# Kernel tuning notes

Measured on AMD Instinct MI355X. Metric: run time of the kernel, lower is better.

The kernel has to match this reference:

```python
import jax, jax.numpy as jnp
import numpy as np

H = W = 32
CROP = int(H * 0.8)  # 25, matches int(H*crop_ratio) in torch
MEAN = jnp.array([0.5071, 0.4867, 0.4408], jnp.float32).reshape(1, 3, 1, 1)
STD = jnp.array([0.2675, 0.2565, 0.2761], jnp.float32).reshape(1, 3, 1, 1)


def _bilinear(img, iy, ix):
    # img [C,H,W]; iy/ix [H,W] float pixel coords (reflected+clamped already)
    y0 = jnp.floor(iy); x0 = jnp.floor(ix)
    wy = iy - y0; wx = ix - x0
    y0i = jnp.clip(y0.astype(jnp.int32), 0, H - 1); y1i = jnp.clip(y0i + 1, 0, H - 1)
    x0i = jnp.clip(x0.astype(jnp.int32), 0, W - 1); x1i = jnp.clip(x0i + 1, 0, W - 1)
    v00 = img[:, y0i, x0i]; v01 = img[:, y0i, x1i]
    v10 = img[:, y1i, x0i]; v11 = img[:, y1i, x1i]
    return v00 * (1 - wy) * (1 - wx) + v01 * (1 - wy) * wx + v10 * wy * (1 - wx) + v11 * wy * wx


def _reflect(c, size):
    # PyTorch grid_sample reflection padding, align_corners=False (reflect about -0.5 / size-0.5)
    lo = -0.5
    span = float(size)
    t = jnp.abs(c - lo)
    extra = jnp.mod(t, span)
    flips = jnp.floor(t / span)
    out = jnp.where(jnp.mod(flips, 2.0) == 0.0, lo + extra, lo + span - extra)
    return jnp.clip(out, 0.0, size - 1.0)


def _crop_resize_one(img, top, left):
    # bilinear resize of img[:, top:top+CROP, left:left+CROP] -> HxW, align_corners=False
    d = (jnp.arange(W, dtype=jnp.float32) + 0.5) * (CROP / W) - 0.5
    d = jnp.maximum(d, 0.0)
    i0 = jnp.floor(d).astype(jnp.int32)
    lam = d - i0
    i1 = jnp.minimum(i0 + 1, CROP - 1)
    r0 = top + i0; r1 = top + i1; c0 = left + i0; c1 = left + i1
    v00 = img[:, r0[:, None], c0[None, :]]
    v01 = img[:, r0[:, None], c1[None, :]]
    v10 = img[:, r1[:, None], c0[None, :]]
    v11 = img[:, r1[:, None], c1[None, :]]
    ly = lam[:, None]; lx = lam[None, :]
    return v00 * (1 - ly) * (1 - lx) + v01 * (1 - ly) * lx + v10 * ly * (1 - lx) + v11 * ly * lx


def _grid_sample_one(img, theta):
    # affine_grid + grid_sample (bilinear, reflection, align_corners=False)
    xs = (2.0 * (jnp.arange(W, dtype=jnp.float32) + 0.5) / W) - 1.0
    ys = (2.0 * (jnp.arange(H, dtype=jnp.float32) + 0.5) / H) - 1.0
    yn, xn = jnp.meshgrid(ys, xs, indexing='ij')
    gx = theta[0, 0] * xn + theta[0, 1] * yn + theta[0, 2]
    gy = theta[1, 0] * xn + theta[1, 1] * yn + theta[1, 2]
    ix = _reflect(((gx + 1.0) * W - 1.0) * 0.5, W)
    iy = _reflect(((gy + 1.0) * H - 1.0) * 0.5, H)
    return _bilinear(img, iy, ix)


def _augment(x, shared_affine, apply_crop):
    B = x.shape[0]
    ks = jax.random.split(jax.random.key(42), 10)
    x = x * STD + MEAN  # de-normalize
    if apply_crop:
        max_off = H - CROP
        top = jax.random.randint(ks[0], (B,), 0, max_off + 1)
        left = jax.random.randint(ks[1], (B,), 0, max_off + 1)
        x = jax.vmap(_crop_resize_one)(x, top, left)
    flip_mask = jax.random.uniform(ks[2], (B,)) < 0.5
    x = jnp.where(flip_mask[:, None, None, None], x[..., ::-1], x)
    # shared affine is provided -> always applied (torch shared_affine branch)
    x = jax.vmap(_grid_sample_one)(x, shared_affine)
    brightness = 1.0 + (jax.random.uniform(ks[3], (B, 1, 1, 1)) - 0.5) * 0.8
    x = x * brightness
    gray = x.mean(axis=1, keepdims=True)
    contrast = 1.0 + (jax.random.uniform(ks[4], (B, 1, 1, 1)) - 0.5) * 0.8
    x = gray + (x - gray) * contrast
    gray = x.mean(axis=1, keepdims=True)
    saturation = 1.0 + (jax.random.uniform(ks[5], (B, 1, 1, 1)) - 0.5) * 0.8
    x = gray + (x - gray) * saturation
    hue_mask = jax.random.uniform(ks[6], (B,)) < 0.5
    x = jnp.where(hue_mask[:, None, None, None], x[:, ::-1], x)  # BGR swap
    gray_mask = jax.random.uniform(ks[7], (B,)) < 0.2
    x = jnp.where(gray_mask[:, None, None, None], x.mean(axis=1, keepdims=True), x)
    blur_mask = jax.random.uniform(ks[8], (B,)) < 0.5
    xp = jnp.pad(x, ((0, 0), (0, 0), (1, 1), (1, 1)), mode='edge')  # replicate pad
    bl = sum(xp[:, :, i:i + H, j:j + W] for i in range(3) for j in range(3)) / 9.0  # 3x3 box blur
    x = jnp.where(blur_mask[:, None, None, None], bl, x)
    solar_mask = jax.random.uniform(ks[9], (B,)) < 0.1
    x = jnp.where(solar_mask[:, None, None, None] & (x > 0.5), 1.0 - x, x)
    x = jnp.clip(x, 0.0, 1.0)
    x = (x - MEAN) / STD  # re-normalize
    return x, flip_mask


def setup_inputs() -> dict:
    key = jax.random.key(0)
    k1, k2 = jax.random.split(key)
    B = 8192
    x = jax.random.normal(k1, (B, 3, H, W), jnp.float32)
    eye = jnp.broadcast_to(jnp.array([[1.0, 0.0, 0.0], [0.0, 1.0, 0.0]], jnp.float32), (B, 2, 3))
    shared_affine = eye + 0.1 * jax.random.normal(k2, (B, 2, 3), jnp.float32)
    return {"x": x, "shared_affine": shared_affine, "apply_crop": 1}


def reference(x, shared_affine, apply_crop):
    out, flip_mask = _augment(x, shared_affine, int(apply_crop))
    # torch returns (x, {'flip': flip_mask, 'affine': affine_theta})
    return out, flip_mask, shared_affine
```

## Files before the change

kernel.cpp:

```cpp
#include <hip/hip_runtime.h>

#define HW 32
#define NPIX 1024
#define IMG 3072

typedef float vf4 __attribute__((ext_vector_type(4)));

__device__ __forceinline__ unsigned rotl32(unsigned x, int d) {
    return (x << d) | (x >> (32 - d));
}

struct UPair { unsigned a, b; };

__device__ __forceinline__ UPair threefry2x32(unsigned k0, unsigned k1,
                                              unsigned x0, unsigned x1) {
    unsigned k2 = k0 ^ k1 ^ 0x1BD11BDAu;
    x0 += k0; x1 += k1;
#define RND(r) { x0 += x1; x1 = rotl32(x1, (r)); x1 ^= x0; }
    RND(13) RND(15) RND(26) RND(6)
    x0 += k1; x1 += k2 + 1u;
    RND(17) RND(29) RND(16) RND(24)
    x0 += k2; x1 += k0 + 2u;
    RND(13) RND(15) RND(26) RND(6)
    x0 += k0; x1 += k1 + 3u;
    RND(17) RND(29) RND(16) RND(24)
    x0 += k1; x1 += k2 + 4u;
    RND(13) RND(15) RND(26) RND(6)
    x0 += k2; x1 += k0 + 5u;
#undef RND
    return {x0, x1};
}

__device__ __forceinline__ float bits_to_u01(unsigned bits) {
    return __uint_as_float((bits >> 9) | 0x3f800000u) - 1.0f;
}

__device__ __forceinline__ float reflect32(float c) {
    float t = fabsf(c + 0.5f);
    float flips = floorf(t * 0.03125f);
    float extra = fmaf(flips, -32.0f, t);
    float o = (((int)flips) & 1) ? (31.5f - extra) : (extra - 0.5f);
    return fminf(fmaxf(o, 0.0f), 31.0f);
}

__device__ __forceinline__ float rfl_f(float v) {
    return __uint_as_float(__builtin_amdgcn_readfirstlane(__float_as_uint(v)));
}
__device__ __forceinline__ int rfl_i(int v) {
    return __builtin_amdgcn_readfirstlane(v);
}

__global__ __launch_bounds__(256) void aug_kernel(
    const float* __restrict__ xin, const float* __restrict__ aff,
    const int* __restrict__ apply_crop, float* __restrict__ out, int B) {
    __shared__ vf4 buf[NPIX];
    __shared__ float s_theta[6];
    __shared__ int s_top, s_left, s_flip, s_hue, s_gray, s_blur, s_solar;
    __shared__ float s_bright, s_contr, s_sat;

    const int b = blockIdx.x;
    const int t = threadIdx.x;
    const int x = t & 31;
    const int yr = t >> 5;
    const bool do_crop = (apply_crop[0] != 0);

    const float* src = xin + (size_t)b * IMG;
    float g0[4], g1[4], g2[4];
#pragma unroll
    for (int i = 0; i < 4; ++i) {
        int p = t + 256 * i;
        g0[i] = src[p];
        g1[i] = src[NPIX + p];
        g2[i] = src[2 * NPIX + p];
    }

    const size_t OUT_IMG = (size_t)B * IMG;
    if (t < 6) {
        float v = aff[b * 6 + t];
        s_theta[t] = v;
        out[OUT_IMG + (size_t)B + (size_t)b * 6 + t] = v;
    }

    if (t < 10) {
        int k = t;
        UPair K = threefry2x32(0u, 42u, 0u, (unsigned)k);
        if (k < 2) {
            UPair k2 = threefry2x32(K.a, K.b, 0u, 1u);
            UPair r = threefry2x32(k2.a, k2.b, 0u, (unsigned)b);
            int val = (int)((r.a ^ r.b) & 7u);
            if (k == 0) s_top = val; else s_left = val;
        } else {
            UPair r = threefry2x32(K.a, K.b, 0u, (unsigned)b);
            float u = bits_to_u01(r.a ^ r.b);
            if      (k == 2) s_flip  = (u < 0.5f);
            else if (k == 3) s_bright = 1.0f + (u - 0.5f) * 0.8f;
            else if (k == 4) s_contr  = 1.0f + (u - 0.5f) * 0.8f;
            else if (k == 5) s_sat    = 1.0f + (u - 0.5f) * 0.8f;
            else if (k == 6) s_hue   = (u < 0.5f);
            else if (k == 7) s_gray  = (u < 0.2f);
            else if (k == 8) s_blur  = (u < 0.5f);
            else             s_solar = (u < 0.1f);
        }
    }

#pragma unroll
    for (int i = 0; i < 4; ++i) {
        vf4 v;
        v.x = fmaf(g0[i], 0.2675f, 0.5071f);
        v.y = fmaf(g1[i], 0.2565f, 0.4867f);
        v.z = fmaf(g2[i], 0.2761f, 0.4408f);
        v.w = 0.0f;
        buf[t + 256 * i] = v;
    }
    __syncthreads();

    if (t == 0) out[OUT_IMG + b] = s_flip ? 1.0f : 0.0f;
    const int top  = rfl_i(s_top),  left = rfl_i(s_left);
    const int flip = rfl_i(s_flip), hue  = rfl_i(s_hue);
    const int gray = rfl_i(s_gray), blur = rfl_i(s_blur), solar = rfl_i(s_solar);
    const float br   = rfl_f(s_bright);
    const float ctsa = rfl_f(s_contr) * rfl_f(s_sat);
    const float th0 = rfl_f(s_theta[0]), th1 = rfl_f(s_theta[1]), th2 = rfl_f(s_theta[2]);
    const float th3 = rfl_f(s_theta[3]), th4 = rfl_f(s_theta[4]), th5 = rfl_f(s_theta[5]);

    float cx[4], cy[4], cz[4];

    if (do_crop) {
        float dxv = fmaxf(fmaf((float)x, 0.78125f, -0.109375f), 0.0f);
        int q0 = (int)dxv; float lx = dxv - (float)q0; int q1 = min(q0 + 1, 24);
        int c0 = left + q0, c1 = left + q1;
        float omx = 1.0f - lx;
#pragma unroll
        for (int i = 0; i < 4; ++i) {
            int yi = yr + 8 * i;
            float dy = fmaxf(fmaf((float)yi, 0.78125f, -0.109375f), 0.0f);
            int i0 = (int)dy; float ly = dy - (float)i0; int i1 = min(i0 + 1, 24);
            int r0 = (top + i0) << 5, r1 = (top + i1) << 5;
            float omy = 1.0f - ly;
            float w00 = omy * omx, w01 = omy * lx;
            float w10 = ly * omx, w11 = ly * lx;
            vf4 t00 = buf[r0 + c0], t01 = buf[r0 + c1];
            vf4 t10 = buf[r1 + c0], t11 = buf[r1 + c1];
            cx[i] = fmaf(t00.x, w00, fmaf(t01.x, w01, fmaf(t10.x, w10, t11.x * w11)));
            cy[i] = fmaf(t00.y, w00, fmaf(t01.y, w01, fmaf(t10.y, w10, t11.y * w11)));
            cz[i] = fmaf(t00.z, w00, fmaf(t01.z, w01, fmaf(t10.z, w10, t11.z * w11)));
        }
        __syncthreads();
#pragma unroll
        for (int i = 0; i < 4; ++i) {
            vf4 v; v.x = cx[i]; v.y = cy[i]; v.z = cz[i]; v.w = 0.0f;
            buf[t + 256 * i] = v;
        }
        __syncthreads();
    }

    {
        float xn = (float)x * 0.0625f - 0.96875f;
#pragma unroll
        for (int i = 0; i < 4; ++i) {
            int yi = yr + 8 * i;
            float yn = (float)yi * 0.0625f - 0.96875f;
            float gx = fmaf(th0, xn, fmaf(th1, yn, th2));
            float gy = fmaf(th3, xn, fmaf(th4, yn, th5));
            float ix = reflect32(fmaf(gx, 16.0f, 15.5f));
            float iy = reflect32(fmaf(gy, 16.0f, 15.5f));
            float fy = floorf(iy), fx = floorf(ix);
            float wy = iy - fy, wx = ix - fx;
            int y0 = (int)fy; int y1 = min(y0 + 1, 31);
            int x0 = (int)fx; int x1 = min(x0 + 1, 31);
            if (flip) { x0 = 31 - x0; x1 = 31 - x1; }
            int r0 = y0 << 5, r1 = y1 << 5;
            float omy = 1.0f - wy, omx = 1.0f - wx;
            float w00 = omy * omx, w01 = omy * wx;
            float w10 = wy * omx, w11 = wy * wx;
            vf4 t00 = buf[r0 + x0], t01 = buf[r0 + x1];
            vf4 t10 = buf[r1 + x0], t11 = buf[r1 + x1];
            float ch0 = fmaf(t00.x, w00, fmaf(t01.x, w01, fmaf(t10.x, w10, t11.x * w11)));
            float ch1 = fmaf(t00.y, w00, fmaf(t01.y, w01, fmaf(t10.y, w10, t11.y * w11)));
            float ch2 = fmaf(t00.z, w00, fmaf(t01.z, w01, fmaf(t10.z, w10, t11.z * w11)));
            ch0 *= br; ch1 *= br; ch2 *= br;
            float g = (ch0 + ch1 + ch2) * (1.0f / 3.0f);
            ch0 = fmaf(ch0 - g, ctsa, g);
            ch1 = fmaf(ch1 - g, ctsa, g);
            ch2 = fmaf(ch2 - g, ctsa, g);
            if (hue) { float tmp = ch0; ch0 = ch2; ch2 = tmp; }
            if (gray) { ch0 = ch1 = ch2 = g; }
            cx[i] = ch0; cy[i] = ch1; cz[i] = ch2;
        }
    }

    if (blur) {
        __syncthreads();
        const int tl = t - 1, tr = t + 1;
        float hx[4], hy[4], hz[4];
#pragma unroll
        for (int i = 0; i < 4; ++i) {
            float v, lf, rt;
            v = cx[i]; lf = __shfl(v, tl); rt = __shfl(v, tr);
            if (x == 0) lf = v;  if (x == 31) rt = v;
            hx[i] = lf + v + rt;
            v = cy[i]; lf = __shfl(v, tl); rt = __shfl(v, tr);
            if (x == 0) lf = v;  if (x == 31) rt = v;
            hy[i] = lf + v + rt;
            v = cz[i]; lf = __shfl(v, tl); rt = __shfl(v, tr);
            if (x == 0) lf = v;  if (x == 31) rt = v;
            hz[i] = lf + v + rt;
        }
#pragma unroll
        for (int i = 0; i < 4; ++i) {
            vf4 v; v.x = hx[i]; v.y = hy[i]; v.z = hz[i]; v.w = 0.0f;
            buf[t + 256 * i] = v;
        }
        __syncthreads();
#pragma unroll
        for (int i = 0; i < 4; ++i) {
            int yi = yr + 8 * i;
            vf4 up = buf[(max(yi - 1, 0) << 5) + x];
            vf4 dn = buf[(min(yi + 1, 31) << 5) + x];
            cx[i] = (up.x + hx[i] + dn.x) * (1.0f / 9.0f);
            cy[i] = (up.y + hy[i] + dn.y) * (1.0f / 9.0f);
            cz[i] = (up.z + hz[i] + dn.z) * (1.0f / 9.0f);
        }
    }

    {
        const float INV0 = 1.0f / 0.2675f, INV1 = 1.0f / 0.2565f, INV2 = 1.0f / 0.2761f;
        float* o = out + (size_t)b * IMG;
#pragma unroll
        for (int i = 0; i < 4; ++i) {
            int p = t + 256 * i;
            float r0v = cx[i], r1v = cy[i], r2v = cz[i];
            if (solar) {
                if (r0v > 0.5f) r0v = 1.0f - r0v;
                if (r1v > 0.5f) r1v = 1.0f - r1v;
                if (r2v > 0.5f) r2v = 1.0f - r2v;
            }
            r0v = fminf(fmaxf(r0v, 0.0f), 1.0f);
            r1v = fminf(fmaxf(r1v, 0.0f), 1.0f);
            r2v = fminf(fmaxf(r2v, 0.0f), 1.0f);
            __builtin_nontemporal_store((r0v - 0.5071f) * INV0, o + p);
            __builtin_nontemporal_store((r1v - 0.4867f) * INV1, o + NPIX + p);
            __builtin_nontemporal_store((r2v - 0.4408f) * INV2, o + 2 * NPIX + p);
        }
    }
}

extern "C" void kernel_launch(void* const* d_in, const int* in_sizes, int n_in,
                              void* d_out, int out_size, void* d_ws, size_t ws_size,
                              hipStream_t stream) {
    const float* x = (const float*)d_in[0];
    const float* aff = (const float*)d_in[1];
    const int* ac = (const int*)d_in[2];
    float* out = (float*)d_out;
    int B = in_sizes[0] / IMG;
    aug_kernel<<<dim3(B), dim3(256), 0, stream>>>(x, aff, ac, out, B);
}
```

Measured before the change: 180.6 us.

## Process four images per block with register prefetch of the next image

Each block now handles four consecutive images in a loop and loads the next image into registers while the current one is processed, so global load latency is hidden. Per-image RNG parameters are computed per wave and broadcast with shuffles instead of going through shared memory, and the crop and grid coordinate constants are hoisted out of the image loop. In exchange the grid shrinks to a quarter of its former size, which lowers the number of waves in flight, and each image still pays for several block barriers.

Result: slower. 206.1 us (+14.1%).

```diff
diff --git a/kernel.cpp b/kernel.cpp
--- a/kernel.cpp
+++ b/kernel.cpp
@@ -3,6 +3,7 @@
 #define HW 32
 #define NPIX 1024
 #define IMG 3072
+#define IPB 4
 
 typedef float vf4 __attribute__((ext_vector_type(4)));
 
@@ -43,125 +44,130 @@
     return fminf(fmaxf(o, 0.0f), 31.0f);
 }
 
-__device__ __forceinline__ float rfl_f(float v) {
-    return __uint_as_float(__builtin_amdgcn_readfirstlane(__float_as_uint(v)));
-}
-__device__ __forceinline__ int rfl_i(int v) {
-    return __builtin_amdgcn_readfirstlane(v);
-}
-
 __global__ __launch_bounds__(256) void aug_kernel(
     const float* __restrict__ xin, const float* __restrict__ aff,
     const int* __restrict__ apply_crop, float* __restrict__ out, int B) {
     __shared__ vf4 buf[NPIX];
-    __shared__ float s_theta[6];
-    __shared__ int s_top, s_left, s_flip, s_hue, s_gray, s_blur, s_solar;
-    __shared__ float s_bright, s_contr, s_sat;
-
-    const int b = blockIdx.x;
+
     const int t = threadIdx.x;
     const int x = t & 31;
     const int yr = t >> 5;
+    const int lane = t & 63;
     const bool do_crop = (apply_crop[0] != 0);
-
-    const float* src = xin + (size_t)b * IMG;
+    const size_t OUT_IMG = (size_t)B * IMG;
+    const int img0 = blockIdx.x * IPB;
+
+    float dxv = fmaxf(fmaf((float)x, 0.78125f, -0.109375f), 0.0f);
+    const int q0c = (int)dxv; const float lxc = dxv - (float)q0c;
+    const int q1c = min(q0c + 1, 24);
+    const float omxc = 1.0f - lxc;
+    const float xn = (float)x * 0.0625f - 0.96875f;
+    int i0a[4], i1a[4]; float lya[4], yna[4];
+#pragma unroll
+    for (int i = 0; i < 4; ++i) {
+        int yi = yr + 8 * i;
+        float dy = fmaxf(fmaf((float)yi, 0.78125f, -0.109375f), 0.0f);
+        i0a[i] = (int)dy; lya[i] = dy - (float)i0a[i];
+        i1a[i] = min(i0a[i] + 1, 24);
+        yna[i] = (float)yi * 0.0625f - 0.96875f;
+    }
+
     float g0[4], g1[4], g2[4];
-#pragma unroll
-    for (int i = 0; i < 4; ++i) {
-        int p = t + 256 * i;
-        g0[i] = src[p];
-        g1[i] = src[NPIX + p];
-        g2[i] = src[2 * NPIX + p];
+    {
+        const float* src = xin + (size_t)img0 * IMG;
+#pragma unroll
+        for (int i = 0; i < 4; ++i) {
+            int p = t + 256 * i;
+            g0[i] = src[p]; g1[i] = src[NPIX + p]; g2[i] = src[2 * NPIX + p];
+        }
     }
 
-    const size_t OUT_IMG = (size_t)B * IMG;
-    if (t < 6) {
-        float v = aff[b * 6 + t];
-        s_theta[t] = v;
-        out[OUT_IMG + (size_t)B + (size_t)b * 6 + t] = v;
-    }
-
-    if (t < 10) {
-        int k = t;
-        UPair K = threefry2x32(0u, 42u, 0u, (unsigned)k);
-        if (k < 2) {
-            UPair k2 = threefry2x32(K.a, K.b, 0u, 1u);
-            UPair r = threefry2x32(k2.a, k2.b, 0u, (unsigned)b);
-            int val = (int)((r.a ^ r.b) & 7u);
-            if (k == 0) s_top = val; else s_left = val;
-        } else {
-            UPair r = threefry2x32(K.a, K.b, 0u, (unsigned)b);
-            float u = bits_to_u01(r.a ^ r.b);
-            if      (k == 2) s_flip  = (u < 0.5f);
-            else if (k == 3) s_bright = 1.0f + (u - 0.5f) * 0.8f;
-            else if (k == 4) s_contr  = 1.0f + (u - 0.5f) * 0.8f;
-            else if (k == 5) s_sat    = 1.0f + (u - 0.5f) * 0.8f;
-            else if (k == 6) s_hue   = (u < 0.5f);
-            else if (k == 7) s_gray  = (u < 0.2f);
-            else if (k == 8) s_blur  = (u < 0.5f);
-            else             s_solar = (u < 0.1f);
-        }
-    }
-
-#pragma unroll
-    for (int i = 0; i < 4; ++i) {
-        vf4 v;
-        v.x = fmaf(g0[i], 0.2675f, 0.5071f);
-        v.y = fmaf(g1[i], 0.2565f, 0.4867f);
-        v.z = fmaf(g2[i], 0.2761f, 0.4408f);
-        v.w = 0.0f;
-        buf[t + 256 * i] = v;
-    }
-    __syncthreads();
-
-    if (t == 0) out[OUT_IMG + b] = s_flip ? 1.0f : 0.0f;
-    const int top  = rfl_i(s_top),  left = rfl_i(s_left);
-    const int flip = rfl_i(s_flip), hue  = rfl_i(s_hue);
-    const int gray = rfl_i(s_gray), blur = rfl_i(s_blur), solar = rfl_i(s_solar);
-    const float br   = rfl_f(s_bright);
-    const float ctsa = rfl_f(s_contr) * rfl_f(s_sat);
-    const float th0 = rfl_f(s_theta[0]), th1 = rfl_f(s_theta[1]), th2 = rfl_f(s_theta[2]);
-    const float th3 = rfl_f(s_theta[3]), th4 = rfl_f(s_theta[4]), th5 = rfl_f(s_theta[5]);
-
-    float cx[4], cy[4], cz[4];
-
-    if (do_crop) {
-        float dxv = fmaxf(fmaf((float)x, 0.78125f, -0.109375f), 0.0f);
-        int q0 = (int)dxv; float lx = dxv - (float)q0; int q1 = min(q0 + 1, 24);
-        int c0 = left + q0, c1 = left + q1;
-        float omx = 1.0f - lx;
+    for (int k = 0; k < IPB; ++k) {
+        const int b = img0 + k;
+        if (b >= B) break;
+
+        float fval = 0.0f; int ival = 0;
+        if (lane < 10) {
+            UPair K = threefry2x32(0u, 42u, 0u, (unsigned)lane);
+            if (lane < 2) {
+                UPair k2 = threefry2x32(K.a, K.b, 0u, 1u);
+                UPair r = threefry2x32(k2.a, k2.b, 0u, (unsigned)b);
+                ival = (int)((r.a ^ r.b) & 7u);
+            } else {
+                UPair r = threefry2x32(K.a, K.b, 0u, (unsigned)b);
+                float u = bits_to_u01(r.a ^ r.b);
+                if      (lane == 2) ival = (u < 0.5f);
+                else if (lane == 3) fval = 1.0f + (u - 0.5f) * 0.8f;
+                else if (lane == 4) fval = 1.0f + (u - 0.5f) * 0.8f;
+                else if (lane == 5) fval = 1.0f + (u - 0.5f) * 0.8f;
+                else if (lane == 6) ival = (u < 0.5f);
+                else if (lane == 7) ival = (u < 0.2f);
+                else if (lane == 8) ival = (u < 0.5f);
+                else                ival = (u < 0.1f);
+            }
+        }
+        const int top  = __shfl(ival, 0), left = __shfl(ival, 1);
+        const int flip = __shfl(ival, 2), hue  = __shfl(ival, 6);
+        const int gray = __shfl(ival, 7), blur = __shfl(ival, 8);
+        const int solar = __shfl(ival, 9);
+        const float br   = __shfl(fval, 3);
+        const float ctsa = __shfl(fval, 4) * __shfl(fval, 5);
+        const float th0 = aff[b * 6 + 0], th1 = aff[b * 6 + 1], th2 = aff[b * 6 + 2];
+        const float th3 = aff[b * 6 + 3], th4 = aff[b * 6 + 4], th5 = aff[b * 6 + 5];
+
 #pragma unroll
         for (int i = 0; i < 4; ++i) {
-            int yi = yr + 8 * i;
-            float dy = fmaxf(fmaf((float)yi, 0.78125f, -0.109375f), 0.0f);
-            int i0 = (int)dy; float ly = dy - (float)i0; int i1 = min(i0 + 1, 24);
-            int r0 = (top + i0) << 5, r1 = (top + i1) << 5;
-            float omy = 1.0f - ly;
-            float w00 = omy * omx, w01 = omy * lx;
-            float w10 = ly * omx, w11 = ly * lx;
-            vf4 t00 = buf[r0 + c0], t01 = buf[r0 + c1];
-            vf4 t10 = buf[r1 + c0], t11 = buf[r1 + c1];
-            cx[i] = fmaf(t00.x, w00, fmaf(t01.x, w01, fmaf(t10.x, w10, t11.x * w11)));
-            cy[i] = fmaf(t00.y, w00, fmaf(t01.y, w01, fmaf(t10.y, w10, t11.y * w11)));
-            cz[i] = fmaf(t00.z, w00, fmaf(t01.z, w01, fmaf(t10.z, w10, t11.z * w11)));
-        }
+            vf4 v;
+            v.x = fmaf(g0[i], 0.2675f, 0.5071f);
+            v.y = fmaf(g1[i], 0.2565f, 0.4867f);
+            v.z = fmaf(g2[i], 0.2761f, 0.4408f);
+            v.w = 0.0f;
+            buf[t + 256 * i] = v;
+        }
+
+        if (k + 1 < IPB && b + 1 < B) {
+            const float* src = xin + (size_t)(b + 1) * IMG;
+#pragma unroll
+            for (int i = 0; i < 4; ++i) {
+                int p = t + 256 * i;
+                g0[i] = src[p]; g1[i] = src[NPIX + p]; g2[i] = src[2 * NPIX + p];
+            }
+        }
+
+        if (t == 0) out[OUT_IMG + b] = flip ? 1.0f : 0.0f;
+        if (t < 6)  out[OUT_IMG + (size_t)B + (size_t)b * 6 + t] = aff[b * 6 + t];
+
         __syncthreads();
+
+        float cx[4], cy[4], cz[4];
+
+        if (do_crop) {
+            const int c0 = left + q0c, c1 = left + q1c;
+#pragma unroll
+            for (int i = 0; i < 4; ++i) {
+                int r0 = (top + i0a[i]) << 5, r1 = (top + i1a[i]) << 5;
+                float ly = lya[i], omy = 1.0f - ly;
+                float w00 = omy * omxc, w01 = omy * lxc;
+                float w10 = ly * omxc, w11 = ly * lxc;
+                vf4 t00 = buf[r0 + c0], t01 = buf[r0 + c1];
+                vf4 t10 = buf[r1 + c0], t11 = buf[r1 + c1];
+                cx[i] = fmaf(t00.x, w00, fmaf(t01.x, w01, fmaf(t10.x, w10, t11.x * w11)));
+                cy[i] = fmaf(t00.y, w00, fmaf(t01.y, w01, fmaf(t10.y, w10, t11.y * w11)));
+                cz[i] = fmaf(t00.z, w00, fmaf(t01.z, w01, fmaf(t10.z, w10, t11.z * w11)));
+            }
+            __syncthreads();
+#pragma unroll
+            for (int i = 0; i < 4; ++i) {
+                vf4 v; v.x = cx[i]; v.y = cy[i]; v.z = cz[i]; v.w = 0.0f;
+                buf[t + 256 * i] = v;
+            }
+            __syncthreads();
+        }
+
 #pragma unroll
         for (int i = 0; i < 4; ++i) {
-            vf4 v; v.x = cx[i]; v.y = cy[i]; v.z = cz[i]; v.w = 0.0f;
-            buf[t + 256 * i] = v;
-        }
-        __syncthreads();
-    }
-
-    {
-        float xn = (float)x * 0.0625f - 0.96875f;
-#pragma unroll
-        for (int i = 0; i < 4; ++i) {
-            int yi = yr + 8 * i;
-            float yn = (float)yi * 0.0625f - 0.96875f;
-            float gx = fmaf(th0, xn, fmaf(th1, yn, th2));
-            float gy = fmaf(th3, xn, fmaf(th4, yn, th5));
+            float gx = fmaf(th0, xn, fmaf(th1, yna[i], th2));
+            float gy = fmaf(th3, xn, fmaf(th4, yna[i], th5));
             float ix = reflect32(fmaf(gx, 16.0f, 15.5f));
             float iy = reflect32(fmaf(gy, 16.0f, 15.5f));
             float fy = floorf(iy), fx = floorf(ix);
@@ -187,61 +193,63 @@
             if (gray) { ch0 = ch1 = ch2 = g; }
             cx[i] = ch0; cy[i] = ch1; cz[i] = ch2;
         }
-    }
-
-    if (blur) {
-        __syncthreads();
-        const int tl = t - 1, tr = t + 1;
-        float hx[4], hy[4], hz[4];
-#pragma unroll
-        for (int i = 0; i < 4; ++i) {
-            float v, lf, rt;
-            v = cx[i]; lf = __shfl(v, tl); rt = __shfl(v, tr);
-            if (x == 0) lf = v;  if (x == 31) rt = v;
-            hx[i] = lf + v + rt;
-            v = cy[i]; lf = __shfl(v, tl); rt = __shfl(v, tr);
-            if (x == 0) lf = v;  if (x == 31) rt = v;
-            hy[i] = lf + v + rt;
-            v = cz[i]; lf = __shfl(v, tl); rt = __shfl(v, tr);
-            if (x == 0) lf = v;  if (x == 31) rt = v;
-            hz[i] = lf + v + rt;
-        }
-#pragma unroll
-        for (int i = 0; i < 4; ++i) {
-            vf4 v; v.x = hx[i]; v.y = hy[i]; v.z = hz[i]; v.w = 0.0f;
-            buf[t + 256 * i] = v;
-        }
-        __syncthreads();
-#pragma unroll
-        for (int i = 0; i < 4; ++i) {
-            int yi = yr + 8 * i;
-            vf4 up = buf[(max(yi - 1, 0) << 5) + x];
-            vf4 dn = buf[(min(yi + 1, 31) << 5) + x];
-            cx[i] = (up.x + hx[i] + dn.x) * (1.0f / 9.0f);
-            cy[i] = (up.y + hy[i] + dn.y) * (1.0f / 9.0f);
-            cz[i] = (up.z + hz[i] + dn.z) * (1.0f / 9.0f);
-        }
-    }
-
-    {
-        const float INV0 = 1.0f / 0.2675f, INV1 = 1.0f / 0.2565f, INV2 = 1.0f / 0.2761f;
-        float* o = out + (size_t)b * IMG;
-#pragma unroll
-        for (int i = 0; i < 4; ++i) {
-            int p = t + 256 * i;
-            float r0v = cx[i], r1v = cy[i], r2v = cz[i];
-            if (solar) {
-                if (r0v > 0.5f) r0v = 1.0f - r0v;
-                if (r1v > 0.5f) r1v = 1.0f - r1v;
-                if (r2v > 0.5f) r2v = 1.0f - r2v;
-            }
-            r0v = fminf(fmaxf(r0v, 0.0f), 1.0f);
-            r1v = fminf(fmaxf(r1v, 0.0f), 1.0f);
-            r2v = fminf(fmaxf(r2v, 0.0f), 1.0f);
-            __builtin_nontemporal_store((r0v - 0.5071f) * INV0, o + p);
-            __builtin_nontemporal_store((r1v - 0.4867f) * INV1, o + NPIX + p);
-            __builtin_nontemporal_store((r2v - 0.4408f) * INV2, o + 2 * NPIX + p);
-        }
+
+        if (blur) {
+            __syncthreads();
+            const int tl = t - 1, tr = t + 1;
+            float hx[4], hy[4], hz[4];
+#pragma unroll
+            for (int i = 0; i < 4; ++i) {
+                float v, lf, rt;
+                v = cx[i]; lf = __shfl(v, tl); rt = __shfl(v, tr);
+                if (x == 0) lf = v;  if (x == 31) rt = v;
+                hx[i] = lf + v + rt;
+                v = cy[i]; lf = __shfl(v, tl); rt = __shfl(v, tr);
+                if (x == 0) lf = v;  if (x == 31) rt = v;
+                hy[i] = lf + v + rt;
+                v = cz[i]; lf = __shfl(v, tl); rt = __shfl(v, tr);
+                if (x == 0) lf = v;  if (x == 31) rt = v;
+                hz[i] = lf + v + rt;
+            }
+#pragma unroll
+            for (int i = 0; i < 4; ++i) {
+                vf4 v; v.x = hx[i]; v.y = hy[i]; v.z = hz[i]; v.w = 0.0f;
+                buf[t + 256 * i] = v;
+            }
+            __syncthreads();
+#pragma unroll
+            for (int i = 0; i < 4; ++i) {
+                int yi = yr + 8 * i;
+                vf4 up = buf[(max(yi - 1, 0) << 5) + x];
+                vf4 dn = buf[(min(yi + 1, 31) << 5) + x];
+                cx[i] = (up.x + hx[i] + dn.x) * (1.0f / 9.0f);
+                cy[i] = (up.y + hy[i] + dn.y) * (1.0f / 9.0f);
+                cz[i] = (up.z + hz[i] + dn.z) * (1.0f / 9.0f);
+            }
+        }
+
+        {
+            const float INV0 = 1.0f / 0.2675f, INV1 = 1.0f / 0.2565f, INV2 = 1.0f / 0.2761f;
+            float* o = out + (size_t)b * IMG;
+#pragma unroll
+            for (int i = 0; i < 4; ++i) {
+                int p = t + 256 * i;
+                float r0v = cx[i], r1v = cy[i], r2v = cz[i];
+                if (solar) {
+                    if (r0v > 0.5f) r0v = 1.0f - r0v;
+                    if (r1v > 0.5f) r1v = 1.0f - r1v;
+                    if (r2v > 0.5f) r2v = 1.0f - r2v;
+                }
+                r0v = fminf(fmaxf(r0v, 0.0f), 1.0f);
+                r1v = fminf(fmaxf(r1v, 0.0f), 1.0f);
+                r2v = fminf(fmaxf(r2v, 0.0f), 1.0f);
+                __builtin_nontemporal_store((r0v - 0.5071f) * INV0, o + p);
+                __builtin_nontemporal_store((r1v - 0.4867f) * INV1, o + NPIX + p);
+                __builtin_nontemporal_store((r2v - 0.4408f) * INV2, o + 2 * NPIX + p);
+            }
+        }
+
+        if (k + 1 < IPB && b + 1 < B) __syncthreads();
     }
 }
 
@@ -253,5 +261,6 @@
     const int* ac = (const int*)d_in[2];
     float* out = (float*)d_out;
     int B = in_sizes[0] / IMG;
-    aug_kernel<<<dim3(B), dim3(256), 0, stream>>>(x, aff, ac, out, B);
-}
+    int grid = (B + IPB - 1) / IPB;
+    aug_kernel<<<dim3(grid), dim3(256), 0, stream>>>(x, aff, ac, out, B);
+}
```
